# Performance work log

Hardware: AMD Instinct MI355X
Metric: run time of the kernel (lower is better)

Reference implementation:

```python
import jax, jax.numpy as jnp
import numpy as np

B = 65536
H = 1024          # hidden_dimension
D_OUT = 2         # output_dimension
N_EXPERTS = 10


def setup_inputs() -> dict:
    key = jax.random.key(0)
    ks = jax.random.split(key, 9)
    s = 0.02
    return {
        "x": jax.random.normal(ks[0], (B, 12), dtype=jnp.float32),
        "W1": jax.random.normal(ks[1], (H, 1), dtype=jnp.float32) * s,    # fc1 weight [out,in]
        "b1": jax.random.normal(ks[2], (H,), dtype=jnp.float32) * s,
        "Wmeta": jax.random.normal(ks[3], (N_EXPERTS, H), dtype=jnp.float32) * s,  # row i = fc_meta[i].weight[:,0]
        "bmeta": jax.random.normal(ks[4], (N_EXPERTS, H), dtype=jnp.float32) * s,  # row i = fc_meta[i].bias
        "W2": jax.random.normal(ks[5], (H, H), dtype=jnp.float32) * s,
        "b2": jax.random.normal(ks[6], (H,), dtype=jnp.float32) * s,
        "W3": jax.random.normal(ks[7], (D_OUT, H), dtype=jnp.float32) * s,
        "b3": jax.random.normal(ks[8], (D_OUT,), dtype=jnp.float32) * s,
    }


def reference(x, W1, b1, Wmeta, bmeta, W2, b2, W3, b3):
    one_hot = x[:, 0:10]          # [B, 10] expert selection weights
    delta = x[:, 10:11]           # [B, 1]
    phi = x[:, 11:12]             # [B, 1]
    # fc1(delta): [B,1] @ [1,H]
    x1 = delta * W1[:, 0] + b1    # [B, H]
    # expert i output: phi * Wmeta[i] + bmeta[i]; one-hot weighted sum over experts
    # sum_i one_hot[:,i]*(phi*Wmeta[i]+bmeta[i]) = phi*(one_hot@Wmeta) + one_hot@bmeta
    x2 = phi * (one_hot @ Wmeta) + one_hot @ bmeta  # [B, H]
    h = jax.nn.relu(x1 + x2)
    h = jax.nn.relu(h @ W2.T + b2)                  # fc2 + relu
    return h @ W3.T + b3                            # fc3 -> [B, 2]
```

## Files before the change

### kernel.cpp

```cpp
#include <hip/hip_runtime.h>
#include <stdint.h>

#define NROWS 65536
#define HD 1024

typedef __attribute__((ext_vector_type(8))) short bf16x8;
typedef __attribute__((ext_vector_type(16))) float f32x16;

typedef __attribute__((address_space(1))) const unsigned int* gas_ptr;
typedef __attribute__((address_space(3))) unsigned int* las_ptr;

__device__ __forceinline__ unsigned short f2bf(float f) {
  union { float f; uint32_t u; } v; v.f = f;
  uint32_t u = v.u;
  return (unsigned short)((u + 0x7fffu + ((u >> 16) & 1u)) >> 16);
}

__device__ __forceinline__ void gl16(const void* g, void* l) {
  __builtin_amdgcn_global_load_lds((gas_ptr)g, (las_ptr)l, 16, 0, 0);
}

__global__ void k_w2bf(const float* __restrict__ W2, unsigned short* __restrict__ W2bf) {
  int i = blockIdx.x * 256 + threadIdx.x;
  int c = i >> 7, g = i & 127;
  const float4* s4 = (const float4*)(W2 + (size_t)c * HD + g * 8);
  float4 a = s4[0], b = s4[1];
  uint4 pk;
  pk.x = (uint32_t)f2bf(a.x) | ((uint32_t)f2bf(a.y) << 16);
  pk.y = (uint32_t)f2bf(a.z) | ((uint32_t)f2bf(a.w) << 16);
  pk.z = (uint32_t)f2bf(b.x) | ((uint32_t)f2bf(b.y) << 16);
  pk.w = (uint32_t)f2bf(b.z) | ((uint32_t)f2bf(b.w) << 16);
  int gs = (g & 124) | ((g & 3) ^ ((c >> 1) & 3));
  *(uint4*)(W2bf + (size_t)c * HD + gs * 8) = pk;
}

__global__ __launch_bounds__(512) void k_layer1(
    const float* __restrict__ x, const float* __restrict__ W1,
    const float* __restrict__ b1, const float* __restrict__ Wmeta,
    const float* __restrict__ bmeta, unsigned short* __restrict__ h) {
  __shared__ float xs[128 * 12];
  int r0 = blockIdx.x * 128;
  int t = threadIdx.x;
  int j0 = t * 2;
  float w1a = W1[j0], w1b = W1[j0 + 1];
  float b1a = b1[j0], b1b = b1[j0 + 1];
  float wma[10], wmb[10], bma[10], bmb[10];
#pragma unroll
  for (int e = 0; e < 10; e++) {
    float2 wmv = *(const float2*)(Wmeta + e * HD + j0);
    float2 bmv = *(const float2*)(bmeta + e * HD + j0);
    wma[e] = wmv.x; wmb[e] = wmv.y; bma[e] = bmv.x; bmb[e] = bmv.y;
  }
  for (int i = t; i < 128 * 12; i += 512) xs[i] = x[(size_t)r0 * 12 + i];
  __syncthreads();
  int g = j0 >> 3;
  for (int r = 0; r < 128; r++) {
    const float* xr = xs + r * 12;
    float delta = xr[10], phi = xr[11];
    float s1a = 0.f, s1b = 0.f, s2a = 0.f, s2b = 0.f;
#pragma unroll
    for (int e = 0; e < 10; e++) {
      float oh = xr[e];
      s1a = fmaf(oh, wma[e], s1a);
      s1b = fmaf(oh, wmb[e], s1b);
      s2a = fmaf(oh, bma[e], s2a);
      s2b = fmaf(oh, bmb[e], s2b);
    }
    float pa = fmaf(delta, w1a, b1a) + fmaf(phi, s1a, s2a);
    float pb = fmaf(delta, w1b, b1b) + fmaf(phi, s1b, s2b);
    pa = fmaxf(pa, 0.f); pb = fmaxf(pb, 0.f);
    uint32_t pk = (uint32_t)f2bf(pa) | ((uint32_t)f2bf(pb) << 16);
    int rr = r0 + r;
    int gs = (g & 124) | ((g & 3) ^ ((rr >> 1) & 3));
    *(uint32_t*)(h + (size_t)rr * HD + gs * 8 + (j0 & 7)) = pk;
  }
}

__global__ __launch_bounds__(256, 3) void k_gemm(
    const unsigned short* __restrict__ h, const unsigned short* __restrict__ W2bf,
    const float* __restrict__ b2, const float* __restrict__ W3,
    float* __restrict__ partial) {
  __shared__ char lds[34816];
  int tid = threadIdx.x;
  int b = (int)blockIdx.x;
  int bx = ((b & 7) << 9) | (b >> 3);
  int rt = bx >> 3, ct = bx & 7;
  size_t r0 = (size_t)rt * 128;
  int c0 = ct * 128;
  int w = tid >> 6, lane = tid & 63;
  int wm = w >> 1, wn = w & 1;
  int l31 = lane & 31, hi = lane >> 5;
  int sw = (l31 >> 1) & 3;

  f32x16 acc[2][2];
#pragma unroll
  for (int rb = 0; rb < 2; rb++)
#pragma unroll
    for (int cb = 0; cb < 2; cb++)
#pragma unroll
      for (int i = 0; i < 16; i++) acc[rb][cb][i] = 0.f;

  int arow0 = (wm * 64 + 0  + l31) * 64;
  int arow1 = (wm * 64 + 32 + l31) * 64;
  int brow0 = (wn * 64 + 0  + l31) * 64;
  int brow1 = (wn * 64 + 32 + l31) * 64;

  for (int T = 0; T < 16; T++) {
#pragma unroll
    for (int q = 0; q < 2; q++) {
      int s = tid + 256 * q;
      int row = s >> 2, g4 = s & 3;
      const unsigned short* hsrc = h    + (r0 + row) * (size_t)HD + T * 64 + g4 * 8;
      const unsigned short* wsrc = W2bf + (size_t)(c0 + row) * HD + T * 64 + g4 * 8;
      gl16(hsrc,      lds +         (size_t)s * 16);
      gl16(hsrc + 32, lds +  8192 + (size_t)s * 16);
      gl16(wsrc,      lds + 16384 + (size_t)s * 16);
      gl16(wsrc + 32, lds + 24576 + (size_t)s * 16);
    }
    __syncthreads();
#pragma unroll
    for (int p = 0; p < 2; p++) {
      const char* lA = lds + p * 8192;
      const char* lB = lds + 16384 + p * 8192;
#pragma unroll
      for (int kl = 0; kl < 2; kl++) {
        int slot = ((kl * 2 + hi) ^ sw) << 4;
        bf16x8 a0 = *(const bf16x8*)(lA + arow0 + slot);
        bf16x8 a1 = *(const bf16x8*)(lA + arow1 + slot);
        bf16x8 b0 = *(const bf16x8*)(lB + brow0 + slot);
        bf16x8 b1 = *(const bf16x8*)(lB + brow1 + slot);
        acc[0][0] = __builtin_amdgcn_mfma_f32_32x32x16_bf16(a0, b0, acc[0][0], 0, 0, 0);
        acc[0][1] = __builtin_amdgcn_mfma_f32_32x32x16_bf16(a0, b1, acc[0][1], 0, 0, 0);
        acc[1][0] = __builtin_amdgcn_mfma_f32_32x32x16_bf16(a1, b0, acc[1][0], 0, 0, 0);
        acc[1][1] = __builtin_amdgcn_mfma_f32_32x32x16_bf16(a1, b1, acc[1][1], 0, 0, 0);
      }
    }
    __syncthreads();
  }

  float b2c[2], w30[2], w31[2];
#pragma unroll
  for (int cb = 0; cb < 2; cb++) {
    int c = c0 + wn * 64 + cb * 32 + l31;
    b2c[cb] = b2[c];
    w30[cb] = W3[c];
    w31[cb] = W3[HD + c];
  }
  float2* sE = (float2*)lds;
#pragma unroll
  for (int rb = 0; rb < 2; rb++) {
    __syncthreads();
#pragma unroll
    for (int reg = 0; reg < 16; reg++) {
      float v0 = fmaxf(acc[rb][0][reg] + b2c[0], 0.f);
      float v1 = fmaxf(acc[rb][1][reg] + b2c[1], 0.f);
      float2 o;
      o.x = v0 * w30[0] + v1 * w30[1];
      o.y = v0 * w31[0] + v1 * w31[1];
      int rowf = (reg & 3) + 8 * (reg >> 2) + 4 * hi;
      int line = (wm * 32 + rowf) * 2 + wn;
      sE[line * 33 + l31] = o;
    }
    __syncthreads();
    int half = tid & 1, tgt = tid >> 1;
    int d = tgt & 1, rowf_t = (tgt >> 1) & 31, bi = tgt >> 6;
    int line0 = (bi * 32 + rowf_t) * 2 + half;
    const float* sf = (const float*)lds;
    float s = 0.f;
#pragma unroll
    for (int j = 0; j < 32; j++) s += sf[(line0 * 33 + j) * 2 + d];
    s += __shfl_xor(s, 1);
    if (half == 0) {
      int row = bi * 64 + rb * 32 + rowf_t;
      partial[(size_t)ct * (NROWS * 2) + (r0 + row) * 2 + d] = s;
    }
  }
}

__global__ void k_reduce(const float* __restrict__ partial, const float* __restrict__ b3,
                         float* __restrict__ out) {
  int i = blockIdx.x * 256 + threadIdx.x;
  float s = b3[i & 1];
#pragma unroll
  for (int ctt = 0; ctt < 8; ctt++) s += partial[(size_t)ctt * 131072 + i];
  out[i] = s;
}

extern "C" void kernel_launch(void* const* d_in, const int* in_sizes, int n_in,
                              void* d_out, int out_size, void* d_ws, size_t ws_size,
                              hipStream_t stream) {
  const float* x     = (const float*)d_in[0];
  const float* W1    = (const float*)d_in[1];
  const float* b1    = (const float*)d_in[2];
  const float* Wmeta = (const float*)d_in[3];
  const float* bmeta = (const float*)d_in[4];
  const float* W2    = (const float*)d_in[5];
  const float* b2    = (const float*)d_in[6];
  const float* W3    = (const float*)d_in[7];
  const float* b3    = (const float*)d_in[8];
  float* out = (float*)d_out;

  char* ws = (char*)d_ws;
  unsigned short* hbuf  = (unsigned short*)ws;
  unsigned short* W2bf  = (unsigned short*)(ws + (size_t)NROWS * HD * 2);
  float* partial = (float*)(ws + (size_t)NROWS * HD * 2 + (size_t)HD * HD * 2);

  k_w2bf<<<512, 256, 0, stream>>>(W2, W2bf);
  k_layer1<<<512, 512, 0, stream>>>(x, W1, b1, Wmeta, bmeta, hbuf);
  k_gemm<<<4096, 256, 0, stream>>>(hbuf, W2bf, b2, W3, partial);
  k_reduce<<<512, 256, 0, stream>>>(partial, b3, out);
}
```

Baseline: 208.7 us.

## Triple-buffer GEMM K-loop with async global-to-LDS prefetch two stages ahead

Rewrites the fc2 GEMM main loop to use a 3-slot LDS ring with 32-wide K tiles, issuing global_load_lds for tile T+2 while tile T is computed. Manual vmcnt waits and a single barrier per iteration replace the two syncthreads per 64-wide tile. It also raises MFMA priority with s_setprio. The aim is to hide global memory latency behind MFMA work. In exchange LDS use grows to 48KB, which may limit occupancy below the launch-bounds target of 3 blocks, and the hand-written waitcnt logic is fragile.

Measured after the change: 225.1 us. +7.8%, slower.

```diff
diff --git a/kernel.cpp b/kernel.cpp
--- a/kernel.cpp
+++ b/kernel.cpp
@@ -3,6 +3,7 @@
 
 #define NROWS 65536
 #define HD 1024
+#define KT 32
 
 typedef __attribute__((ext_vector_type(8))) short bf16x8;
 typedef __attribute__((ext_vector_type(16))) float f32x16;
@@ -80,7 +81,7 @@
     const unsigned short* __restrict__ h, const unsigned short* __restrict__ W2bf,
     const float* __restrict__ b2, const float* __restrict__ W3,
     float* __restrict__ partial) {
-  __shared__ char lds[34816];
+  __shared__ char lds[49152];
   int tid = threadIdx.x;
   int b = (int)blockIdx.x;
   int bx = ((b & 7) << 9) | (b >> 3);
@@ -91,6 +92,8 @@
   int wm = w >> 1, wn = w & 1;
   int l31 = lane & 31, hi = lane >> 5;
   int sw = (l31 >> 1) & 3;
+  int g0 = (hi ^ sw) << 4;
+  int g1 = ((2 + hi) ^ sw) << 4;
 
   f32x16 acc[2][2];
 #pragma unroll
@@ -100,42 +103,51 @@
 #pragma unroll
       for (int i = 0; i < 16; i++) acc[rb][cb][i] = 0.f;
 
-  int arow0 = (wm * 64 + 0  + l31) * 64;
-  int arow1 = (wm * 64 + 32 + l31) * 64;
-  int brow0 = (wn * 64 + 0  + l31) * 64;
-  int brow1 = (wn * 64 + 32 + l31) * 64;
-
-  for (int T = 0; T < 16; T++) {
+  int arow0 = (wm * 64 + l31) * 64;
+  int brow0 = (wn * 64 + l31) * 64;
+
+  auto stage = [&](int T) {
+    char* base = lds + (T % 3) * 16384;
 #pragma unroll
     for (int q = 0; q < 2; q++) {
-      int s = tid + 256 * q;
-      int row = s >> 2, g4 = s & 3;
-      const unsigned short* hsrc = h    + (r0 + row) * (size_t)HD + T * 64 + g4 * 8;
-      const unsigned short* wsrc = W2bf + (size_t)(c0 + row) * HD + T * 64 + g4 * 8;
-      gl16(hsrc,      lds +         (size_t)s * 16);
-      gl16(hsrc + 32, lds +  8192 + (size_t)s * 16);
-      gl16(wsrc,      lds + 16384 + (size_t)s * 16);
-      gl16(wsrc + 32, lds + 24576 + (size_t)s * 16);
-    }
-    __syncthreads();
-#pragma unroll
-    for (int p = 0; p < 2; p++) {
-      const char* lA = lds + p * 8192;
-      const char* lB = lds + 16384 + p * 8192;
-#pragma unroll
-      for (int kl = 0; kl < 2; kl++) {
-        int slot = ((kl * 2 + hi) ^ sw) << 4;
-        bf16x8 a0 = *(const bf16x8*)(lA + arow0 + slot);
-        bf16x8 a1 = *(const bf16x8*)(lA + arow1 + slot);
-        bf16x8 b0 = *(const bf16x8*)(lB + brow0 + slot);
-        bf16x8 b1 = *(const bf16x8*)(lB + brow1 + slot);
-        acc[0][0] = __builtin_amdgcn_mfma_f32_32x32x16_bf16(a0, b0, acc[0][0], 0, 0, 0);
-        acc[0][1] = __builtin_amdgcn_mfma_f32_32x32x16_bf16(a0, b1, acc[0][1], 0, 0, 0);
-        acc[1][0] = __builtin_amdgcn_mfma_f32_32x32x16_bf16(a1, b0, acc[1][0], 0, 0, 0);
-        acc[1][1] = __builtin_amdgcn_mfma_f32_32x32x16_bf16(a1, b1, acc[1][1], 0, 0, 0);
-      }
-    }
-    __syncthreads();
+      int idx = tid + 256 * q;
+      int row = idx >> 2, g4 = idx & 3;
+      gl16(h    + (r0 + row) * (size_t)HD + T * 32 + g4 * 8, base +        (size_t)idx * 16);
+      gl16(W2bf + (size_t)(c0 + row) * HD + T * 32 + g4 * 8, base + 8192 + (size_t)idx * 16);
+    }
+  };
+
+  stage(0); stage(1);
+  asm volatile("s_waitcnt vmcnt(4)" ::: "memory");
+  __builtin_amdgcn_s_barrier();
+
+  for (int T = 0; T < KT; T++) {
+    const char* lA = lds + (T % 3) * 16384;
+    const char* lB = lA + 8192;
+    bf16x8 a00 = *(const bf16x8*)(lA + arow0 + g0);
+    bf16x8 a01 = *(const bf16x8*)(lA + arow0 + g1);
+    bf16x8 a10 = *(const bf16x8*)(lA + arow0 + 2048 + g0);
+    bf16x8 a11 = *(const bf16x8*)(lA + arow0 + 2048 + g1);
+    bf16x8 b00 = *(const bf16x8*)(lB + brow0 + g0);
+    bf16x8 b01 = *(const bf16x8*)(lB + brow0 + g1);
+    bf16x8 b10 = *(const bf16x8*)(lB + brow0 + 2048 + g0);
+    bf16x8 b11 = *(const bf16x8*)(lB + brow0 + 2048 + g1);
+    if (T < KT - 2) stage(T + 2);
+    asm volatile("s_waitcnt lgkmcnt(0)" ::: "memory");
+    __builtin_amdgcn_sched_barrier(0);
+    __builtin_amdgcn_s_setprio(1);
+    acc[0][0] = __builtin_amdgcn_mfma_f32_32x32x16_bf16(a00, b00, acc[0][0], 0, 0, 0);
+    acc[0][1] = __builtin_amdgcn_mfma_f32_32x32x16_bf16(a00, b10, acc[0][1], 0, 0, 0);
+    acc[1][0] = __builtin_amdgcn_mfma_f32_32x32x16_bf16(a10, b00, acc[1][0], 0, 0, 0);
+    acc[1][1] = __builtin_amdgcn_mfma_f32_32x32x16_bf16(a10, b10, acc[1][1], 0, 0, 0);
+    acc[0][0] = __builtin_amdgcn_mfma_f32_32x32x16_bf16(a01, b01, acc[0][0], 0, 0, 0);
+    acc[0][1] = __builtin_amdgcn_mfma_f32_32x32x16_bf16(a01, b11, acc[0][1], 0, 0, 0);
+    acc[1][0] = __builtin_amdgcn_mfma_f32_32x32x16_bf16(a11, b01, acc[1][0], 0, 0, 0);
+    acc[1][1] = __builtin_amdgcn_mfma_f32_32x32x16_bf16(a11, b11, acc[1][1], 0, 0, 0);
+    __builtin_amdgcn_s_setprio(0);
+    if (T == KT - 2) { asm volatile("s_waitcnt vmcnt(0)" ::: "memory"); }
+    else             { asm volatile("s_waitcnt vmcnt(4)" ::: "memory"); }
+    __builtin_amdgcn_s_barrier();
   }
 
   float b2c[2], w30[2], w31[2];
```

## Load GEMM A operand directly from global to registers, bypass LDS

Applied to the files above, without the earlier changes.

The GEMM kernel now reads its activation (A) fragments straight from global memory into registers and stages only W2 through LDS, halving LDS traffic per k-step. Layer1 writes h unswizzled, since the XOR swizzle was only needed for the LDS layout. Launch bounds change from 3 to 4 blocks per CU, allowing more occupancy. The cost is uncoalesced, strided 16-byte global reads for A, with no LDS sharing of A between the two wn waves, so each A element is fetched twice per block.

Measured after the change: 323.5 us. 55.0% more time.

```diff
diff --git a/kernel.cpp b/kernel.cpp
--- a/kernel.cpp
+++ b/kernel.cpp
@@ -53,7 +53,6 @@
   }
   for (int i = t; i < 128 * 12; i += 512) xs[i] = x[(size_t)r0 * 12 + i];
   __syncthreads();
-  int g = j0 >> 3;
   for (int r = 0; r < 128; r++) {
     const float* xr = xs + r * 12;
     float delta = xr[10], phi = xr[11];
@@ -70,13 +69,11 @@
     float pb = fmaf(delta, w1b, b1b) + fmaf(phi, s1b, s2b);
     pa = fmaxf(pa, 0.f); pb = fmaxf(pb, 0.f);
     uint32_t pk = (uint32_t)f2bf(pa) | ((uint32_t)f2bf(pb) << 16);
-    int rr = r0 + r;
-    int gs = (g & 124) | ((g & 3) ^ ((rr >> 1) & 3));
-    *(uint32_t*)(h + (size_t)rr * HD + gs * 8 + (j0 & 7)) = pk;
-  }
-}
-
-__global__ __launch_bounds__(256, 3) void k_gemm(
+    *(uint32_t*)(h + (size_t)(r0 + r) * HD + j0) = pk;
+  }
+}
+
+__global__ __launch_bounds__(256, 4) void k_gemm(
     const unsigned short* __restrict__ h, const unsigned short* __restrict__ W2bf,
     const float* __restrict__ b2, const float* __restrict__ W3,
     float* __restrict__ partial) {
@@ -100,35 +97,43 @@
 #pragma unroll
       for (int i = 0; i < 16; i++) acc[rb][cb][i] = 0.f;
 
-  int arow0 = (wm * 64 + 0  + l31) * 64;
-  int arow1 = (wm * 64 + 32 + l31) * 64;
   int brow0 = (wn * 64 + 0  + l31) * 64;
   int brow1 = (wn * 64 + 32 + l31) * 64;
+  const unsigned short* aBase = h + (r0 + wm * 64 + l31) * (size_t)HD + hi * 8;
 
   for (int T = 0; T < 16; T++) {
+    const unsigned short* at = aBase + T * 64;
+    bf16x8 a000 = *(const bf16x8*)(at + 0);
+    bf16x8 a001 = *(const bf16x8*)(at + 16);
+    bf16x8 a010 = *(const bf16x8*)(at + 32);
+    bf16x8 a011 = *(const bf16x8*)(at + 48);
+    const unsigned short* at1 = at + 32 * (size_t)HD;
+    bf16x8 a100 = *(const bf16x8*)(at1 + 0);
+    bf16x8 a101 = *(const bf16x8*)(at1 + 16);
+    bf16x8 a110 = *(const bf16x8*)(at1 + 32);
+    bf16x8 a111 = *(const bf16x8*)(at1 + 48);
 #pragma unroll
     for (int q = 0; q < 2; q++) {
       int s = tid + 256 * q;
       int row = s >> 2, g4 = s & 3;
-      const unsigned short* hsrc = h    + (r0 + row) * (size_t)HD + T * 64 + g4 * 8;
       const unsigned short* wsrc = W2bf + (size_t)(c0 + row) * HD + T * 64 + g4 * 8;
-      gl16(hsrc,      lds +         (size_t)s * 16);
-      gl16(hsrc + 32, lds +  8192 + (size_t)s * 16);
-      gl16(wsrc,      lds + 16384 + (size_t)s * 16);
-      gl16(wsrc + 32, lds + 24576 + (size_t)s * 16);
+      gl16(wsrc,      lds +        (size_t)s * 16);
+      gl16(wsrc + 32, lds + 8192 + (size_t)s * 16);
     }
     __syncthreads();
 #pragma unroll
     for (int p = 0; p < 2; p++) {
-      const char* lA = lds + p * 8192;
-      const char* lB = lds + 16384 + p * 8192;
+      const char* lB = lds + p * 8192;
 #pragma unroll
       for (int kl = 0; kl < 2; kl++) {
         int slot = ((kl * 2 + hi) ^ sw) << 4;
-        bf16x8 a0 = *(const bf16x8*)(lA + arow0 + slot);
-        bf16x8 a1 = *(const bf16x8*)(lA + arow1 + slot);
         bf16x8 b0 = *(const bf16x8*)(lB + brow0 + slot);
         bf16x8 b1 = *(const bf16x8*)(lB + brow1 + slot);
+        bf16x8 a0, a1;
+        if (p == 0 && kl == 0) { a0 = a000; a1 = a100; }
+        else if (p == 0)       { a0 = a001; a1 = a101; }
+        else if (kl == 0)      { a0 = a010; a1 = a110; }
+        else                   { a0 = a011; a1 = a111; }
         acc[0][0] = __builtin_amdgcn_mfma_f32_32x32x16_bf16(a0, b0, acc[0][0], 0, 0, 0);
         acc[0][1] = __builtin_amdgcn_mfma_f32_32x32x16_bf16(a0, b1, acc[0][1], 0, 0, 0);
         acc[1][0] = __builtin_amdgcn_mfma_f32_32x32x16_bf16(a1, b0, acc[1][0], 0, 0, 0);
```

## Prepack W2 into MFMA fragment order and load B directly to registers

Applied to the files above, without the earlier changes.

W2 is now converted to bf16 and stored in the exact per-lane MFMA B-fragment order. The GEMM kernel therefore loads B operands straight from global memory into registers instead of staging them through LDS. This halves LDS traffic and the number of async copies per K-step, and the occupancy hint rises from 3 to 4 blocks. It also splits layer1 into twice as many smaller blocks. The cost is that the B loads are now ordinary global loads that sit in the critical path without LDS double-buffering, and they add register pressure.

After: 204.6 us. 2.0% less time.

```diff
diff --git a/kernel.cpp b/kernel.cpp
--- a/kernel.cpp
+++ b/kernel.cpp
@@ -20,26 +20,28 @@
   __builtin_amdgcn_global_load_lds((gas_ptr)g, (las_ptr)l, 16, 0, 0);
 }
 
-__global__ void k_w2bf(const float* __restrict__ W2, unsigned short* __restrict__ W2bf) {
+__global__ void k_w2pk(const float* __restrict__ W2, unsigned short* __restrict__ W2pk) {
   int i = blockIdx.x * 256 + threadIdx.x;
-  int c = i >> 7, g = i & 127;
-  const float4* s4 = (const float4*)(W2 + (size_t)c * HD + g * 8);
+  int lane = i & 63, f = (i >> 6) & 15, T = (i >> 10) & 15, ct = i >> 14;
+  int kl = f & 1, p = (f >> 1) & 1, cb = (f >> 2) & 1, wn = f >> 3;
+  int col = ct * 128 + wn * 64 + cb * 32 + (lane & 31);
+  int k = T * 64 + p * 32 + kl * 16 + (lane >> 5) * 8;
+  const float4* s4 = (const float4*)(W2 + (size_t)col * HD + k);
   float4 a = s4[0], b = s4[1];
   uint4 pk;
   pk.x = (uint32_t)f2bf(a.x) | ((uint32_t)f2bf(a.y) << 16);
   pk.y = (uint32_t)f2bf(a.z) | ((uint32_t)f2bf(a.w) << 16);
   pk.z = (uint32_t)f2bf(b.x) | ((uint32_t)f2bf(b.y) << 16);
   pk.w = (uint32_t)f2bf(b.z) | ((uint32_t)f2bf(b.w) << 16);
-  int gs = (g & 124) | ((g & 3) ^ ((c >> 1) & 3));
-  *(uint4*)(W2bf + (size_t)c * HD + gs * 8) = pk;
+  *(uint4*)(W2pk + (size_t)i * 8) = pk;
 }
 
 __global__ __launch_bounds__(512) void k_layer1(
     const float* __restrict__ x, const float* __restrict__ W1,
     const float* __restrict__ b1, const float* __restrict__ Wmeta,
     const float* __restrict__ bmeta, unsigned short* __restrict__ h) {
-  __shared__ float xs[128 * 12];
-  int r0 = blockIdx.x * 128;
+  __shared__ float xs[64 * 12];
+  int r0 = blockIdx.x * 64;
   int t = threadIdx.x;
   int j0 = t * 2;
   float w1a = W1[j0], w1b = W1[j0 + 1];
@@ -51,10 +53,10 @@
     float2 bmv = *(const float2*)(bmeta + e * HD + j0);
     wma[e] = wmv.x; wmb[e] = wmv.y; bma[e] = bmv.x; bmb[e] = bmv.y;
   }
-  for (int i = t; i < 128 * 12; i += 512) xs[i] = x[(size_t)r0 * 12 + i];
+  for (int i = t; i < 64 * 12; i += 512) xs[i] = x[(size_t)r0 * 12 + i];
   __syncthreads();
   int g = j0 >> 3;
-  for (int r = 0; r < 128; r++) {
+  for (int r = 0; r < 64; r++) {
     const float* xr = xs + r * 12;
     float delta = xr[10], phi = xr[11];
     float s1a = 0.f, s1b = 0.f, s2a = 0.f, s2b = 0.f;
@@ -76,8 +78,8 @@
   }
 }
 
-__global__ __launch_bounds__(256, 3) void k_gemm(
-    const unsigned short* __restrict__ h, const unsigned short* __restrict__ W2bf,
+__global__ __launch_bounds__(256, 4) void k_gemm(
+    const unsigned short* __restrict__ h, const unsigned short* __restrict__ W2pk,
     const float* __restrict__ b2, const float* __restrict__ W3,
     float* __restrict__ partial) {
   __shared__ char lds[34816];
@@ -102,37 +104,37 @@
 
   int arow0 = (wm * 64 + 0  + l31) * 64;
   int arow1 = (wm * 64 + 32 + l31) * 64;
-  int brow0 = (wn * 64 + 0  + l31) * 64;
-  int brow1 = (wn * 64 + 32 + l31) * 64;
+  const unsigned short* bwave = W2pk + ((size_t)ct * 16 * 16 + (size_t)wn * 8) * 512 + lane * 8;
 
   for (int T = 0; T < 16; T++) {
+    const unsigned short* bt = bwave + (size_t)T * 16 * 512;
+    bf16x8 B[2][4];
+#pragma unroll
+    for (int cb = 0; cb < 2; cb++)
+#pragma unroll
+      for (int pk = 0; pk < 4; pk++)
+        B[cb][pk] = *(const bf16x8*)(bt + (cb * 4 + pk) * 512);
 #pragma unroll
     for (int q = 0; q < 2; q++) {
       int s = tid + 256 * q;
       int row = s >> 2, g4 = s & 3;
-      const unsigned short* hsrc = h    + (r0 + row) * (size_t)HD + T * 64 + g4 * 8;
-      const unsigned short* wsrc = W2bf + (size_t)(c0 + row) * HD + T * 64 + g4 * 8;
-      gl16(hsrc,      lds +         (size_t)s * 16);
-      gl16(hsrc + 32, lds +  8192 + (size_t)s * 16);
-      gl16(wsrc,      lds + 16384 + (size_t)s * 16);
-      gl16(wsrc + 32, lds + 24576 + (size_t)s * 16);
+      const unsigned short* hsrc = h + (r0 + row) * (size_t)HD + T * 64 + g4 * 8;
+      gl16(hsrc,      lds +        (size_t)s * 16);
+      gl16(hsrc + 32, lds + 8192 + (size_t)s * 16);
     }
     __syncthreads();
 #pragma unroll
     for (int p = 0; p < 2; p++) {
       const char* lA = lds + p * 8192;
-      const char* lB = lds + 16384 + p * 8192;
 #pragma unroll
       for (int kl = 0; kl < 2; kl++) {
         int slot = ((kl * 2 + hi) ^ sw) << 4;
         bf16x8 a0 = *(const bf16x8*)(lA + arow0 + slot);
         bf16x8 a1 = *(const bf16x8*)(lA + arow1 + slot);
-        bf16x8 b0 = *(const bf16x8*)(lB + brow0 + slot);
-        bf16x8 b1 = *(const bf16x8*)(lB + brow1 + slot);
-        acc[0][0] = __builtin_amdgcn_mfma_f32_32x32x16_bf16(a0, b0, acc[0][0], 0, 0, 0);
-        acc[0][1] = __builtin_amdgcn_mfma_f32_32x32x16_bf16(a0, b1, acc[0][1], 0, 0, 0);
-        acc[1][0] = __builtin_amdgcn_mfma_f32_32x32x16_bf16(a1, b0, acc[1][0], 0, 0, 0);
-        acc[1][1] = __builtin_amdgcn_mfma_f32_32x32x16_bf16(a1, b1, acc[1][1], 0, 0, 0);
+        acc[0][0] = __builtin_amdgcn_mfma_f32_32x32x16_bf16(a0, B[0][p * 2 + kl], acc[0][0], 0, 0, 0);
+        acc[0][1] = __builtin_amdgcn_mfma_f32_32x32x16_bf16(a0, B[1][p * 2 + kl], acc[0][1], 0, 0, 0);
+        acc[1][0] = __builtin_amdgcn_mfma_f32_32x32x16_bf16(a1, B[0][p * 2 + kl], acc[1][0], 0, 0, 0);
+        acc[1][1] = __builtin_amdgcn_mfma_f32_32x32x16_bf16(a1, B[1][p * 2 + kl], acc[1][1], 0, 0, 0);
       }
     }
     __syncthreads();
@@ -202,11 +204,11 @@
 
   char* ws = (char*)d_ws;
   unsigned short* hbuf  = (unsigned short*)ws;
-  unsigned short* W2bf  = (unsigned short*)(ws + (size_t)NROWS * HD * 2);
+  unsigned short* W2pk  = (unsigned short*)(ws + (size_t)NROWS * HD * 2);
   float* partial = (float*)(ws + (size_t)NROWS * HD * 2 + (size_t)HD * HD * 2);
 
-  k_w2bf<<<512, 256, 0, stream>>>(W2, W2bf);
-  k_layer1<<<512, 512, 0, stream>>>(x, W1, b1, Wmeta, bmeta, hbuf);
-  k_gemm<<<4096, 256, 0, stream>>>(hbuf, W2bf, b2, W3, partial);
+  k_w2pk<<<512, 256, 0, stream>>>(W2, W2pk);
+  k_layer1<<<1024, 512, 0, stream>>>(x, W1, b1, Wmeta, bmeta, hbuf);
+  k_gemm<<<4096, 256, 0, stream>>>(hbuf, W2pk, b2, W3, partial);
   k_reduce<<<512, 256, 0, stream>>>(partial, b3, out);
 }
```
